# Kernel tuning notes

Measured on AMD Instinct MI355X. Metric: run time of the kernel, lower is better.

## Reference

```python
import jax, jax.numpy as jnp
import numpy as np

N_RAYS, N_SAMPLES, RES = 4096, 256, 128
RGB_C = 15
XYZ_MIN, XYZ_MAX = -1.0, 1.0
NEAR, FAR, STEPSIZE, BG = 0.2, 3.0, 0.5, 1.0
ALPHA_INIT = 0.01
ACT_SHIFT = float(np.log(1.0 / (1.0 - ALPHA_INIT) - 1.0))
N_FREQ = 6
EMB_DIM = 3 + 3 * 2 * N_FREQ  # 39
DIM0 = RGB_C + EMB_DIM        # 54


def _trilinear(grid, u):
    # grid: [C, R, R, R]; u: [N, 3] normalized to [0,1]; align_corners=True
    R = grid.shape[1]
    pos = jnp.clip(u, 0.0, 1.0) * (R - 1)
    i0 = jnp.clip(jnp.floor(pos).astype(jnp.int32), 0, R - 2)
    f = pos - i0.astype(pos.dtype)
    i1 = i0 + 1
    x0, y0, z0 = i0[:, 0], i0[:, 1], i0[:, 2]
    x1, y1, z1 = i1[:, 0], i1[:, 1], i1[:, 2]
    fx, fy, fz = f[:, 0], f[:, 1], f[:, 2]
    c = (grid[:, x0, y0, z0] * ((1 - fx) * (1 - fy) * (1 - fz))
         + grid[:, x1, y0, z0] * (fx * (1 - fy) * (1 - fz))
         + grid[:, x0, y1, z0] * ((1 - fx) * fy * (1 - fz))
         + grid[:, x0, y0, z1] * ((1 - fx) * (1 - fy) * fz)
         + grid[:, x1, y1, z0] * (fx * fy * (1 - fz))
         + grid[:, x1, y0, z1] * (fx * (1 - fy) * fz)
         + grid[:, x0, y1, z1] * ((1 - fx) * fy * fz)
         + grid[:, x1, y1, z1] * (fx * fy * fz))
    return c.T  # [N, C]


def _embed(x):
    # NeRF positional encoding, multires=6, include inputs: [..., 3] -> [..., 39]
    freqs = 2.0 ** jnp.arange(N_FREQ, dtype=x.dtype)
    xb = x[..., None, :] * freqs[:, None]  # [..., 6, 3]
    shp = x.shape[:-1]
    return jnp.concatenate([x, jnp.sin(xb).reshape(*shp, -1), jnp.cos(xb).reshape(*shp, -1)], -1)


def setup_inputs() -> dict:
    key = jax.random.key(0)
    ks = jax.random.split(key, 12)
    return {
        "rays_o": jax.random.uniform(ks[0], (N_RAYS, 3), minval=-0.5, maxval=0.5),
        "rays_d": jax.random.normal(ks[1], (N_RAYS, 3)),
        "viewdirs": jax.random.normal(ks[2], (N_RAYS, 3)),
        "latent_grid": jax.random.normal(ks[3], (1 + RGB_C, RES, RES, RES)) * 0.1,
        "normals_grid": jax.random.normal(ks[4], (3, RES, RES, RES)),
        "W0": jax.random.normal(ks[5], (DIM0, 64)) * 0.1, "b0": jnp.zeros((64,)),
        "W1": jax.random.normal(ks[6], (64, 64)) * 0.1, "b1": jnp.zeros((64,)),
        "W2": jax.random.normal(ks[7], (64, 64)) * 0.1, "b2": jnp.zeros((64,)),
        "W3": jax.random.normal(ks[8], (64, 3)) * 0.1, "b3": jnp.zeros((3,)),
    }


def reference(rays_o, rays_d, viewdirs, latent_grid, normals_grid,
              W0, b0, W1, b1, W2, b2, W3, b3):
    rays_d = rays_d / jnp.linalg.norm(rays_d, axis=-1, keepdims=True)
    viewdirs = viewdirs / jnp.linalg.norm(viewdirs, axis=-1, keepdims=True)
    # sample_ray: uniform steps along each ray
    t = jnp.linspace(NEAR, FAR, N_SAMPLES, dtype=rays_o.dtype)
    ray_pts = rays_o[:, None, :] + rays_d[:, None, :] * t[None, :, None]  # [R,S,3]
    inbbox = jnp.all((ray_pts >= XYZ_MIN) & (ray_pts <= XYZ_MAX), -1)      # [R,S]
    u = ((ray_pts - XYZ_MIN) / (XYZ_MAX - XYZ_MIN)).reshape(-1, 3)
    lat = _trilinear(latent_grid, u).reshape(N_RAYS, N_SAMPLES, 1 + RGB_C)
    nrm = _trilinear(normals_grid, u).reshape(N_RAYS, N_SAMPLES, 3)
    nrm = nrm / jnp.maximum(jnp.linalg.norm(nrm, axis=-1, keepdims=True), 1e-12)
    nrm = jnp.where(inbbox[..., None], nrm, 0.0)
    density = lat[..., 0]
    # activate_density: 1 - exp(-softplus(d + shift) * interval), zero outside bbox
    alpha = jnp.where(inbbox, 1.0 - jnp.exp(-jax.nn.softplus(density + ACT_SHIFT) * STEPSIZE), 0.0)
    # cumprod_exclusive transmittance
    alphainv_cum = jnp.concatenate(
        [jnp.ones_like(alpha[..., :1]), jnp.cumprod(jnp.clip(1.0 - alpha, 1e-10, None), -1)], -1)
    weights = alpha * alphainv_cum[..., :-1]
    # reflection directions: 2*(-v.n)*n + v
    vde = jnp.broadcast_to(viewdirs[:, None, :], nrm.shape)
    dot = jnp.sum(-vde * nrm, -1, keepdims=True)
    refdirs = 2.0 * dot * nrm + vde
    feat = jnp.concatenate([jnp.where(inbbox[..., None], lat[..., 1:], 0.0), _embed(refdirs)], -1)
    h = jax.nn.relu(feat @ W0 + b0)
    h = jax.nn.relu(h @ W1 + b1)
    h = jax.nn.relu(h @ W2 + b2)
    rgb = jnp.where(inbbox[..., None], jax.nn.sigmoid(h @ W3 + b3), 0.0)
    rgb_marched = jnp.sum(weights[..., None] * rgb, -2) + alphainv_cum[..., -1:] * BG
    depth = jnp.linalg.norm(rays_o[:, None, :] - ray_pts, axis=-1)
    depth_marched = jnp.sum(weights * depth, -1) + alphainv_cum[..., -1] * FAR
    disp = 1.0 / depth_marched
    acc = weights.sum(-1)
    normals_marched = jnp.sum(weights[..., None] * nrm, -2)
    return rgb_marched, depth_marched, disp, acc, normals_marched, weights, alphainv_cum
```

## Files before the change

kernel.cpp:

```cpp
#include <hip/hip_runtime.h>
#include <hip/hip_bf16.h>
#include <math.h>

typedef __hip_bfloat16 bf16;
typedef float f32x4 __attribute__((ext_vector_type(4)));
typedef short short8 __attribute__((ext_vector_type(8)));

#define NRAYS 4096
#define NSAMP 256
#define RESG  128
#define RS2   16384
#define RS3   2097152
#define ACT_SHIFT (-4.59511985013459f)

#define OFLAG 0
#define OBIAS 16
#define ORO   272
#define ORD   12560
#define OVD   24848
#define FRAG_BYTE_OFF 148544
#define LATIL_BYTE_OFF 1048576ULL
#define NRMIL_BYTE_OFF 68157440ULL
#define WS_NEED        101711872ULL

__device__ __forceinline__ float ldT(const float* p, size_t i){ return p[i]; }
__device__ __forceinline__ float ldT(const bf16*  p, size_t i){ return __bfloat162float(p[i]); }

__device__ __forceinline__ unsigned short f2bu(float f){
  unsigned int x = __float_as_uint(f);
  unsigned int r = (x + 0x7FFFu + ((x >> 16) & 1u)) >> 16;
  return (unsigned short)r;
}
__device__ __forceinline__ float bu2f(short s){
  return __uint_as_float(((unsigned int)(unsigned short)s) << 16);
}

template<typename T>
__device__ void fill_ws(const void* W0,const void* b0,const void* W1,const void* b1,
                        const void* W2,const void* b2,const void* W3,const void* b3,
                        const void* ro,const void* rd,const void* vd,
                        float* __restrict__ wb, int tid)
{
  const T* tW0=(const T*)W0; const T* tb0=(const T*)b0;
  const T* tW1=(const T*)W1; const T* tb1=(const T*)b1;
  const T* tW2=(const T*)W2; const T* tb2=(const T*)b2;
  const T* tW3=(const T*)W3; const T* tb3=(const T*)b3;
  const T* tro=(const T*)ro; const T* trd=(const T*)rd; const T* tvd=(const T*)vd;

  for (int idx = tid; idx < 64; idx += 256){
    wb[16+idx]  = ldT(tb0, idx);
    wb[80+idx]  = ldT(tb1, idx);
    wb[144+idx] = ldT(tb2, idx);
  }
  if (tid < 16) wb[224+tid] = (tid < 3) ? ldT(tb3, tid) : 0.0f;

  for (int r = tid; r < NRAYS; r += 256){
    float ox = ldT(tro, r*3+0), oy = ldT(tro, r*3+1), oz = ldT(tro, r*3+2);
    wb[ORO+r*3+0]=ox; wb[ORO+r*3+1]=oy; wb[ORO+r*3+2]=oz;
    float dx = ldT(trd, r*3+0), dy = ldT(trd, r*3+1), dz = ldT(trd, r*3+2);
    float dn = 1.0f / sqrtf(dx*dx+dy*dy+dz*dz);
    wb[ORD+r*3+0]=dx*dn; wb[ORD+r*3+1]=dy*dn; wb[ORD+r*3+2]=dz*dn;
    float vx = ldT(tvd, r*3+0), vy = ldT(tvd, r*3+1), vz = ldT(tvd, r*3+2);
    float vn = 1.0f / sqrtf(vx*vx+vy*vy+vz*vz);
    wb[OVD+r*3+0]=vx*vn; wb[OVD+r*3+1]=vy*vn; wb[OVD+r*3+2]=vz*vn;
  }

  unsigned short* fu = (unsigned short*)((char*)wb + FRAG_BYTE_OFF);
  for (int idx = tid; idx < 4096; idx += 256){
    int blk = idx >> 9, rem = idx & 511, lane = rem >> 3, j = rem & 7;
    int nt = blk >> 1, ks = blk & 1;
    int k = ks*32 + ((lane>>4)<<3) + j, n = nt*16 + (lane & 15);
    float v = (k < 54) ? ldT(tW0, k*64 + n) : 0.0f;
    fu[idx] = f2bu(v);
  }
  for (int idx = tid; idx < 4096; idx += 256){
    int blk = idx >> 9, rem = idx & 511, lane = rem >> 3, j = rem & 7;
    int nt = blk >> 1, ks = blk & 1;
    int k = ks*32 + ((lane>>4)<<3) + j, n = nt*16 + (lane & 15);
    fu[4096+idx] = f2bu(ldT(tW1, k*64 + n));
    fu[8192+idx] = f2bu(ldT(tW2, k*64 + n));
  }
  for (int idx = tid; idx < 1024; idx += 256){
    int blk = idx >> 9, rem = idx & 511, lane = rem >> 3, j = rem & 7;
    int ks = blk;
    int k = ks*32 + ((lane>>4)<<3) + j, n = lane & 15;
    float v = (n < 3) ? ldT(tW3, k*3 + n) : 0.0f;
    fu[12288+idx] = f2bu(v);
  }
}

__global__ void prep(const void* W0,const void* b0,const void* W1,const void* b1,
                     const void* W2,const void* b2,const void* W3,const void* b3,
                     const void* ro,const void* rd,const void* vd,
                     float* __restrict__ wb)
{
  __shared__ int s_f32;
  const int tid = threadIdx.x;
  if (tid == 0) s_f32 = 0;
  __syncthreads();
  {
    const bf16* t1 = (const bf16*)W1;
    float a = fabsf(__bfloat162float(t1[2*tid]));
    float b = fabsf(__bfloat162float(t1[2*tid+1]));
    if (!(a < 100.0f) || !(b < 100.0f)) atomicOr(&s_f32, 1);
  }
  __syncthreads();
  const bool isf32 = (s_f32 != 0);
  if (tid == 0) wb[OFLAG] = isf32 ? 1.0f : 0.0f;
  if (isf32) fill_ws<float>(W0,b0,W1,b1,W2,b2,W3,b3,ro,rd,vd,wb,tid);
  else       fill_ws<bf16 >(W0,b0,W1,b1,W2,b2,W3,b3,ro,rd,vd,wb,tid);
}

__global__ __launch_bounds__(256)
void interleave_lat(const void* __restrict__ latent, float* __restrict__ wb)
{
  unsigned short* lat_il = (unsigned short*)((char*)wb + LATIL_BYTE_OFF);
  const int T = blockIdx.x*256 + threadIdx.x;
  const int v = T >> 1, h = T & 1, cb = h*8;
  short8 o;
  if (wb[OFLAG] > 0.5f){
    const float* p = (const float*)latent;
#pragma unroll
    for (int j = 0; j < 8; j++) o[j] = (short)f2bu(p[(size_t)(cb+j)*RS3 + v]);
  } else {
    const unsigned short* p = (const unsigned short*)latent;
#pragma unroll
    for (int j = 0; j < 8; j++) o[j] = (short)p[(size_t)(cb+j)*RS3 + v];
  }
  *(short8*)&lat_il[((size_t)v<<4) + cb] = o;
}

__global__ __launch_bounds__(256)
void interleave_nrm(const void* __restrict__ normals, float* __restrict__ wb)
{
  f32x4* nrm_il = (f32x4*)((char*)wb + NRMIL_BYTE_OFF);
  const int v = blockIdx.x*256 + threadIdx.x;
  f32x4 o;
  if (wb[OFLAG] > 0.5f){
    const float* p = (const float*)normals;
    o[0]=p[v]; o[1]=p[(size_t)RS3+v]; o[2]=p[(size_t)2*RS3+v]; o[3]=0.0f;
  } else {
    const unsigned short* p = (const unsigned short*)normals;
    o[0]=bu2f(p[v]); o[1]=bu2f(p[(size_t)RS3+v]); o[2]=bu2f(p[(size_t)2*RS3+v]); o[3]=0.0f;
  }
  nrm_il[v] = o;
}

__global__ __launch_bounds__(256, 4)
void render_fast(const float* __restrict__ wb, float* __restrict__ out)
{
  const int ray  = blockIdx.x;
  const int i    = threadIdx.x;
  const int lane = i & 63;
  const int wv   = i >> 6;
  const int quad = lane >> 4;
  const int n15  = lane & 15;
  const int wbase = wv * 64;

  __shared__ unsigned short act[NSAMP*72];
  __shared__ float sh_w[NSAMP];
  __shared__ float sh_wt[4];
  __shared__ float red[4][8];
  __shared__ float red_rgb[4][16];

  const unsigned short* lat_il = (const unsigned short*)((const char*)wb + LATIL_BYTE_OFF);
  const f32x4* nrm_il = (const f32x4*)((const char*)wb + NRMIL_BYTE_OFF);

  const float ox = wb[ORO+ray*3+0], oy = wb[ORO+ray*3+1], oz = wb[ORO+ray*3+2];
  const float dx = wb[ORD+ray*3+0], dy = wb[ORD+ray*3+1], dz = wb[ORD+ray*3+2];
  const float vx = wb[OVD+ray*3+0], vy = wb[OVD+ray*3+1], vz = wb[OVD+ray*3+2];

  const float t  = 0.2f + (2.8f/255.0f) * (float)i;
  const float px = ox + dx*t, py = oy + dy*t, pz = oz + dz*t;
  const bool inb = (px >= -1.0f) & (px <= 1.0f) & (py >= -1.0f) & (py <= 1.0f)
                 & (pz >= -1.0f) & (pz <= 1.0f);

  float alpha = 0.0f, nx = 0.0f, ny = 0.0f, nz = 0.0f;
  unsigned short* arow = &act[i*72];

  if (inb) {
    float ux = fminf(fmaxf((px+1.0f)*0.5f, 0.0f), 1.0f) * 127.0f;
    float uy = fminf(fmaxf((py+1.0f)*0.5f, 0.0f), 1.0f) * 127.0f;
    float uz = fminf(fmaxf((pz+1.0f)*0.5f, 0.0f), 1.0f) * 127.0f;
    int x0 = (int)floorf(ux); x0 = x0 > 126 ? 126 : (x0 < 0 ? 0 : x0);
    int y0 = (int)floorf(uy); y0 = y0 > 126 ? 126 : (y0 < 0 ? 0 : y0);
    int z0 = (int)floorf(uz); z0 = z0 > 126 ? 126 : (z0 < 0 ? 0 : z0);
    float fx = ux - (float)x0, fy = uy - (float)y0, fz = uz - (float)z0;
    const float gx = 1.0f - fx, gy = 1.0f - fy, gz = 1.0f - fz;

    const int vb = (x0<<14) + (y0<<7) + z0;
    const unsigned short* Lp = lat_il + ((size_t)vb<<4);
    const f32x4* Np = nrm_il + vb;

    float ch[16];
#pragma unroll
    for (int c = 0; c < 16; c++) ch[c] = 0.0f;
    float nr0 = 0.0f, nr1 = 0.0f, nr2 = 0.0f;

    const int   loff[4] = {0, 1<<18, 1<<11, (1<<18)+(1<<11)};
    const int   noff[4] = {0, 16384, 128, 16384+128};
    const float wxy[4]  = {gx*gy, fx*gy, gx*fy, fx*fy};

#pragma unroll
    for (int cr = 0; cr < 4; cr++){
      const unsigned short* p = Lp + loff[cr];
      short8 a0 = *(const short8*)(p);
      short8 a1 = *(const short8*)(p+8);
      short8 b0 = *(const short8*)(p+16);
      short8 b1 = *(const short8*)(p+24);
      const float wz0 = wxy[cr]*gz, wz1 = wxy[cr]*fz;
#pragma unroll
      for (int j = 0; j < 8; j++){
        ch[j]   += wz0*bu2f(a0[j]) + wz1*bu2f(b0[j]);
        ch[j+8] += wz0*bu2f(a1[j]) + wz1*bu2f(b1[j]);
      }
      f32x4 n0 = Np[noff[cr]];
      f32x4 n1 = Np[noff[cr]+1];
      nr0 += wz0*n0[0] + wz1*n1[0];
      nr1 += wz0*n0[1] + wz1*n1[1];
      nr2 += wz0*n0[2] + wz1*n1[2];
    }

    float xs = ch[0] + ACT_SHIFT;
    float sp = xs > 15.0f ? xs : log1pf(__expf(xs));
    alpha = 1.0f - __expf(-sp * 0.5f);

    float nn  = sqrtf(nr0*nr0 + nr1*nr1 + nr2*nr2);
    float ninv = 1.0f / fmaxf(nn, 1e-12f);
    nx = nr0*ninv; ny = nr1*ninv; nz = nr2*ninv;

    float dt = -(vx*nx + vy*ny + vz*nz);
    float rx = 2.0f*dt*nx + vx, ry = 2.0f*dt*ny + vy, rz = 2.0f*dt*nz + vz;

    short8 v0, v1;
#pragma unroll
    for (int j = 0; j < 8; j++) v0[j] = (short)f2bu(ch[1+j]);
#pragma unroll
    for (int j = 0; j < 7; j++) v1[j] = (short)f2bu(ch[9+j]);
    v1[7] = (short)f2bu(rx);
    *(short8*)&arow[0] = v0; *(short8*)&arow[8] = v1;
    v0[0]=(short)f2bu(ry); v0[1]=(short)f2bu(rz);
    v0[2]=(short)f2bu(__sinf(rx));        v0[3]=(short)f2bu(__sinf(ry));        v0[4]=(short)f2bu(__sinf(rz));
    v0[5]=(short)f2bu(__sinf(rx*2.0f));   v0[6]=(short)f2bu(__sinf(ry*2.0f));   v0[7]=(short)f2bu(__sinf(rz*2.0f));
    v1[0]=(short)f2bu(__sinf(rx*4.0f));   v1[1]=(short)f2bu(__sinf(ry*4.0f));   v1[2]=(short)f2bu(__sinf(rz*4.0f));
    v1[3]=(short)f2bu(__sinf(rx*8.0f));   v1[4]=(short)f2bu(__sinf(ry*8.0f));   v1[5]=(short)f2bu(__sinf(rz*8.0f));
    v1[6]=(short)f2bu(__sinf(rx*16.0f));  v1[7]=(short)f2bu(__sinf(ry*16.0f));
    *(short8*)&arow[16] = v0; *(short8*)&arow[24] = v1;
    v0[0]=(short)f2bu(__sinf(rz*16.0f));  v0[1]=(short)f2bu(__sinf(rx*32.0f));
    v0[2]=(short)f2bu(__sinf(ry*32.0f));  v0[3]=(short)f2bu(__sinf(rz*32.0f));
    v0[4]=(short)f2bu(__cosf(rx));        v0[5]=(short)f2bu(__cosf(ry));        v0[6]=(short)f2bu(__cosf(rz));
    v0[7]=(short)f2bu(__cosf(rx*2.0f));
    v1[0]=(short)f2bu(__cosf(ry*2.0f));   v1[1]=(short)f2bu(__cosf(rz*2.0f));
    v1[2]=(short)f2bu(__cosf(rx*4.0f));   v1[3]=(short)f2bu(__cosf(ry*4.0f));   v1[4]=(short)f2bu(__cosf(rz*4.0f));
    v1[5]=(short)f2bu(__cosf(rx*8.0f));   v1[6]=(short)f2bu(__cosf(ry*8.0f));   v1[7]=(short)f2bu(__cosf(rz*8.0f));
    *(short8*)&arow[32] = v0; *(short8*)&arow[40] = v1;
    v0[0]=(short)f2bu(__cosf(rx*16.0f));  v0[1]=(short)f2bu(__cosf(ry*16.0f));  v0[2]=(short)f2bu(__cosf(rz*16.0f));
    v0[3]=(short)f2bu(__cosf(rx*32.0f));  v0[4]=(short)f2bu(__cosf(ry*32.0f));  v0[5]=(short)f2bu(__cosf(rz*32.0f));
    v0[6]=0; v0[7]=0;
#pragma unroll
    for (int j = 0; j < 8; j++) v1[j] = 0;
    *(short8*)&arow[48] = v0; *(short8*)&arow[56] = v1;
  } else {
    short8 z;
#pragma unroll
    for (int j = 0; j < 8; j++) z[j] = 0;
#pragma unroll
    for (int c = 0; c < 8; c++) *(short8*)&arow[c*8] = z;
  }

  float xv = fmaxf(1.0f - alpha, 1e-10f);
  float incl = xv;
#pragma unroll
  for (int off = 1; off < 64; off <<= 1){
    float y = __shfl_up(incl, off, 64);
    if (lane >= off) incl *= y;
  }
  float excl = __shfl_up(incl, 1, 64);
  if (lane == 0) excl = 1.0f;
  if (lane == 63) sh_wt[wv] = incl;
  __syncthreads();

  float pre = 1.0f;
#pragma unroll
  for (int k = 0; k < 4; k++) if (k < wv) pre *= sh_wt[k];
  const float last = sh_wt[0]*sh_wt[1]*sh_wt[2]*sh_wt[3];
  const float av = pre * excl;
  const float w  = alpha * av;
  sh_w[i] = w;

  float* outw = out + 36864;
  float* outa = out + 36864 + 1048576;
  outw[ray*NSAMP + i] = w;
  outa[ray*(NSAMP+1) + i] = av;
  if (i == NSAMP-1) outa[ray*(NSAMP+1) + NSAMP] = last;

  {
    float vals[5] = { w*t, w, w*nx, w*ny, w*nz };
#pragma unroll
    for (int v = 0; v < 5; v++){
      float s = vals[v];
#pragma unroll
      for (int m = 32; m > 0; m >>= 1) s += __shfl_xor(s, m, 64);
      if (lane == 0) red[wv][v] = s;
    }
  }
  __syncthreads();
  if (i == 0){
    float s0 = red[0][0]+red[1][0]+red[2][0]+red[3][0];
    float s1 = red[0][1]+red[1][1]+red[2][1]+red[3][1];
    float s2 = red[0][2]+red[1][2]+red[2][2]+red[3][2];
    float s3 = red[0][3]+red[1][3]+red[2][3]+red[3][3];
    float s4 = red[0][4]+red[1][4]+red[2][4]+red[3][4];
    const float dm = s0 + last * 3.0f;
    float* o1 = out + 12288; o1[ray] = dm;
    float* o2 = out + 16384; o2[ray] = 1.0f / dm;
    float* o3 = out + 20480; o3[ray] = s1;
    float* o4 = out + 24576;
    o4[ray*3+0] = s2; o4[ray*3+1] = s3; o4[ray*3+2] = s4;
  }

  const short8* fr = (const short8*)((const char*)wb + FRAG_BYTE_OFF);

#pragma unroll
  for (int l = 0; l < 3; l++){
    const int fbase = l * 512;
    f32x4 acc[4][4];
#pragma unroll
    for (int mt = 0; mt < 4; mt++)
#pragma unroll
      for (int nt = 0; nt < 4; nt++) acc[mt][nt] = (f32x4){0.f,0.f,0.f,0.f};

#pragma unroll
    for (int ks = 0; ks < 2; ks++){
      short8 a[4], b[4];
#pragma unroll
      for (int mt = 0; mt < 4; mt++)
        a[mt] = *(const short8*)&act[(wbase + mt*16 + n15)*72 + ks*32 + quad*8];
#pragma unroll
      for (int nt = 0; nt < 4; nt++)
        b[nt] = fr[fbase + (nt*2+ks)*64 + lane];
#pragma unroll
      for (int mt = 0; mt < 4; mt++)
#pragma unroll
        for (int nt = 0; nt < 4; nt++)
          acc[mt][nt] = __builtin_amdgcn_mfma_f32_16x16x32_bf16(a[mt], b[nt], acc[mt][nt], 0, 0, 0);
    }
    __syncthreads();
#pragma unroll
    for (int nt = 0; nt < 4; nt++){
      const float bn = wb[OBIAS + l*64 + nt*16 + n15];
#pragma unroll
      for (int mt = 0; mt < 4; mt++){
#pragma unroll
        for (int r = 0; r < 4; r++){
          float vv = fmaxf(acc[mt][nt][r] + bn, 0.0f);
          act[(wbase + mt*16 + quad*4 + r)*72 + nt*16 + n15] = f2bu(vv);
        }
      }
    }
    __syncthreads();
  }

  {
    f32x4 acc3[4];
#pragma unroll
    for (int mt = 0; mt < 4; mt++) acc3[mt] = (f32x4){0.f,0.f,0.f,0.f};
#pragma unroll
    for (int ks = 0; ks < 2; ks++){
      short8 a[4];
#pragma unroll
      for (int mt = 0; mt < 4; mt++)
        a[mt] = *(const short8*)&act[(wbase + mt*16 + n15)*72 + ks*32 + quad*8];
      short8 b = fr[1536 + ks*64 + lane];
#pragma unroll
      for (int mt = 0; mt < 4; mt++)
        acc3[mt] = __builtin_amdgcn_mfma_f32_16x16x32_bf16(a[mt], b, acc3[mt], 0, 0, 0);
    }
    const float bn3 = wb[OBIAS + 208 + n15];
    float p = 0.0f;
#pragma unroll
    for (int mt = 0; mt < 4; mt++){
#pragma unroll
      for (int r = 0; r < 4; r++){
        const float wr = sh_w[wbase + mt*16 + quad*4 + r];
        const float logit = acc3[mt][r] + bn3;
        p += wr * (1.0f / (1.0f + __expf(-logit)));
      }
    }
    p += __shfl_xor(p, 16, 64);
    p += __shfl_xor(p, 32, 64);
    if (lane < 16) red_rgb[wv][lane] = p;
  }
  __syncthreads();
  if (i < 3){
    float s = red_rgb[0][i] + red_rgb[1][i] + red_rgb[2][i] + red_rgb[3][i];
    out[ray*3+i] = s + last;
  }
}

template<typename GT>
__device__ __forceinline__ void render_body(const GT* __restrict__ latent,
                                            const GT* __restrict__ normals,
                                            const float* __restrict__ wb,
                                            float* __restrict__ out)
{
  const int ray  = blockIdx.x;
  const int i    = threadIdx.x;
  const int lane = i & 63;
  const int wv   = i >> 6;
  const int quad = lane >> 4;
  const int n15  = lane & 15;
  const int wbase = wv * 64;

  __shared__ unsigned short act[NSAMP*72];
  __shared__ float sh_w[NSAMP];
  __shared__ float sh_wt[4];
  __shared__ float red[4][8];
  __shared__ float red_rgb[4][16];

  const float ox = wb[ORO+ray*3+0], oy = wb[ORO+ray*3+1], oz = wb[ORO+ray*3+2];
  const float dx = wb[ORD+ray*3+0], dy = wb[ORD+ray*3+1], dz = wb[ORD+ray*3+2];
  const float vx = wb[OVD+ray*3+0], vy = wb[OVD+ray*3+1], vz = wb[OVD+ray*3+2];

  const float t  = 0.2f + (2.8f/255.0f) * (float)i;
  const float px = ox + dx*t, py = oy + dy*t, pz = oz + dz*t;
  const bool inb = (px >= -1.0f) & (px <= 1.0f) & (py >= -1.0f) & (py <= 1.0f)
                 & (pz >= -1.0f) & (pz <= 1.0f);

  float alpha = 0.0f, nx = 0.0f, ny = 0.0f, nz = 0.0f;
  float fv[64];
#pragma unroll
  for (int k = 0; k < 64; k++) fv[k] = 0.0f;

  if (inb) {
    float ux = fminf(fmaxf((px+1.0f)*0.5f, 0.0f), 1.0f) * 127.0f;
    float uy = fminf(fmaxf((py+1.0f)*0.5f, 0.0f), 1.0f) * 127.0f;
    float uz = fminf(fmaxf((pz+1.0f)*0.5f, 0.0f), 1.0f) * 127.0f;
    int x0 = (int)floorf(ux); x0 = x0 > 126 ? 126 : (x0 < 0 ? 0 : x0);
    int y0 = (int)floorf(uy); y0 = y0 > 126 ? 126 : (y0 < 0 ? 0 : y0);
    int z0 = (int)floorf(uz); z0 = z0 > 126 ? 126 : (z0 < 0 ? 0 : z0);
    float fx = ux - (float)x0, fy = uy - (float)y0, fz = uz - (float)z0;
    const int base = x0*RS2 + y0*RESG + z0;
    const float gx = 1.0f - fx, gy = 1.0f - fy, gz = 1.0f - fz;
    const float w000 = gx*gy*gz, w100 = fx*gy*gz, w010 = gx*fy*gz, w001 = gx*gy*fz;
    const float w110 = fx*fy*gz, w101 = fx*gy*fz, w011 = gx*fy*fz, w111 = fx*fy*fz;

    float ch[19];
#pragma unroll
    for (int c = 0; c < 19; c++){
      const GT* g = (c < 16 ? latent + c*RS3 : normals + (c-16)*RS3) + base;
      ch[c] = w000*ldT(g,0)        + w100*ldT(g,RS2)
            + w010*ldT(g,RESG)     + w001*ldT(g,1)
            + w110*ldT(g,RS2+RESG) + w101*ldT(g,RS2+1)
            + w011*ldT(g,RESG+1)   + w111*ldT(g,RS2+RESG+1);
    }

    float xs = ch[0] + ACT_SHIFT;
    float sp = xs > 15.0f ? xs : log1pf(__expf(xs));
    alpha = 1.0f - __expf(-sp * 0.5f);

    float nn  = sqrtf(ch[16]*ch[16] + ch[17]*ch[17] + ch[18]*ch[18]);
    float ninv = 1.0f / fmaxf(nn, 1e-12f);
    nx = ch[16]*ninv; ny = ch[17]*ninv; nz = ch[18]*ninv;

    float dt = -(vx*nx + vy*ny + vz*nz);
    float rx = 2.0f*dt*nx + vx, ry = 2.0f*dt*ny + vy, rz = 2.0f*dt*nz + vz;

#pragma unroll
    for (int k = 0; k < 15; k++) fv[k] = ch[k+1];
    fv[15] = rx; fv[16] = ry; fv[17] = rz;
#pragma unroll
    for (int f = 0; f < 6; f++){
      float s = (float)(1 << f);
      fv[18 + f*3 + 0] = __sinf(rx*s);
      fv[18 + f*3 + 1] = __sinf(ry*s);
      fv[18 + f*3 + 2] = __sinf(rz*s);
      fv[36 + f*3 + 0] = __cosf(rx*s);
      fv[36 + f*3 + 1] = __cosf(ry*s);
      fv[36 + f*3 + 2] = __cosf(rz*s);
    }
  }

#pragma unroll
  for (int c = 0; c < 8; c++){
    short8 v;
#pragma unroll
    for (int k = 0; k < 8; k++) v[k] = (short)f2bu(fv[c*8+k]);
    *(short8*)&act[i*72 + c*8] = v;
  }

  float xvv = fmaxf(1.0f - alpha, 1e-10f);
  float incl = xvv;
#pragma unroll
  for (int off = 1; off < 64; off <<= 1){
    float y = __shfl_up(incl, off, 64);
    if (lane >= off) incl *= y;
  }
  float excl = __shfl_up(incl, 1, 64);
  if (lane == 0) excl = 1.0f;
  if (lane == 63) sh_wt[wv] = incl;
  __syncthreads();

  float pre = 1.0f;
#pragma unroll
  for (int k = 0; k < 4; k++) if (k < wv) pre *= sh_wt[k];
  const float last = sh_wt[0]*sh_wt[1]*sh_wt[2]*sh_wt[3];
  const float av = pre * excl;
  const float w  = alpha * av;
  sh_w[i] = w;

  float* outw = out + 36864;
  float* outa = out + 36864 + 1048576;
  outw[ray*NSAMP + i] = w;
  outa[ray*(NSAMP+1) + i] = av;
  if (i == NSAMP-1) outa[ray*(NSAMP+1) + NSAMP] = last;

  {
    float vals[5] = { w*t, w, w*nx, w*ny, w*nz };
#pragma unroll
    for (int v = 0; v < 5; v++){
      float s = vals[v];
#pragma unroll
      for (int m = 32; m > 0; m >>= 1) s += __shfl_xor(s, m, 64);
      if (lane == 0) red[wv][v] = s;
    }
  }
  __syncthreads();
  if (i == 0){
    float s0 = red[0][0]+red[1][0]+red[2][0]+red[3][0];
    float s1 = red[0][1]+red[1][1]+red[2][1]+red[3][1];
    float s2 = red[0][2]+red[1][2]+red[2][2]+red[3][2];
    float s3 = red[0][3]+red[1][3]+red[2][3]+red[3][3];
    float s4 = red[0][4]+red[1][4]+red[2][4]+red[3][4];
    const float dm = s0 + last * 3.0f;
    float* o1 = out + 12288; o1[ray] = dm;
    float* o2 = out + 16384; o2[ray] = 1.0f / dm;
    float* o3 = out + 20480; o3[ray] = s1;
    float* o4 = out + 24576;
    o4[ray*3+0] = s2; o4[ray*3+1] = s3; o4[ray*3+2] = s4;
  }

  const short8* fr = (const short8*)((const char*)wb + FRAG_BYTE_OFF);

#pragma unroll
  for (int l = 0; l < 3; l++){
    const int fbase = l * 512;
    f32x4 acc[4][4];
#pragma unroll
    for (int mt = 0; mt < 4; mt++)
#pragma unroll
      for (int nt = 0; nt < 4; nt++) acc[mt][nt] = (f32x4){0.f,0.f,0.f,0.f};

#pragma unroll
    for (int ks = 0; ks < 2; ks++){
      short8 a[4], b[4];
#pragma unroll
      for (int mt = 0; mt < 4; mt++)
        a[mt] = *(const short8*)&act[(wbase + mt*16 + n15)*72 + ks*32 + quad*8];
#pragma unroll
      for (int nt = 0; nt < 4; nt++)
        b[nt] = fr[fbase + (nt*2+ks)*64 + lane];
#pragma unroll
      for (int mt = 0; mt < 4; mt++)
#pragma unroll
        for (int nt = 0; nt < 4; nt++)
          acc[mt][nt] = __builtin_amdgcn_mfma_f32_16x16x32_bf16(a[mt], b[nt], acc[mt][nt], 0, 0, 0);
    }
    __syncthreads();
#pragma unroll
    for (int nt = 0; nt < 4; nt++){
      const float bn = wb[OBIAS + l*64 + nt*16 + n15];
#pragma unroll
      for (int mt = 0; mt < 4; mt++){
#pragma unroll
        for (int r = 0; r < 4; r++){
          float vv = fmaxf(acc[mt][nt][r] + bn, 0.0f);
          act[(wbase + mt*16 + quad*4 + r)*72 + nt*16 + n15] = f2bu(vv);
        }
      }
    }
    __syncthreads();
  }

  {
    f32x4 acc3[4];
#pragma unroll
    for (int mt = 0; mt < 4; mt++) acc3[mt] = (f32x4){0.f,0.f,0.f,0.f};
#pragma unroll
    for (int ks = 0; ks < 2; ks++){
      short8 a[4];
#pragma unroll
      for (int mt = 0; mt < 4; mt++)
        a[mt] = *(const short8*)&act[(wbase + mt*16 + n15)*72 + ks*32 + quad*8];
      short8 b = fr[1536 + ks*64 + lane];
#pragma unroll
      for (int mt = 0; mt < 4; mt++)
        acc3[mt] = __builtin_amdgcn_mfma_f32_16x16x32_bf16(a[mt], b, acc3[mt], 0, 0, 0);
    }
    const float bn3 = wb[OBIAS + 208 + n15];
    float p = 0.0f;
#pragma unroll
    for (int mt = 0; mt < 4; mt++){
#pragma unroll
      for (int r = 0; r < 4; r++){
        const float wr = sh_w[wbase + mt*16 + quad*4 + r];
        const float logit = acc3[mt][r] + bn3;
        p += wr * (1.0f / (1.0f + __expf(-logit)));
      }
    }
    p += __shfl_xor(p, 16, 64);
    p += __shfl_xor(p, 32, 64);
    if (lane < 16) red_rgb[wv][lane] = p;
  }
  __syncthreads();
  if (i < 3){
    float s = red_rgb[0][i] + red_rgb[1][i] + red_rgb[2][i] + red_rgb[3][i];
    out[ray*3+i] = s + last;
  }
}

__global__ __launch_bounds__(256)
void render_fallback(const void* __restrict__ latent, const void* __restrict__ normals,
                     const float* __restrict__ wb, float* __restrict__ out)
{
  if (wb[OFLAG] > 0.5f)
    render_body<float>((const float*)latent, (const float*)normals, wb, out);
  else
    render_body<bf16 >((const bf16*)latent,  (const bf16*)normals,  wb, out);
}

extern "C" void kernel_launch(void* const* d_in, const int* in_sizes, int n_in,
                              void* d_out, int out_size, void* d_ws, size_t ws_size,
                              hipStream_t stream)
{
  float* wb = (float*)d_ws;
  prep<<<1, 256, 0, stream>>>(d_in[5], d_in[6], d_in[7], d_in[8],
                              d_in[9], d_in[10], d_in[11], d_in[12],
                              d_in[0], d_in[1], d_in[2], wb);
  if (ws_size >= WS_NEED){
    interleave_lat<<<16384, 256, 0, stream>>>(d_in[3], wb);
    interleave_nrm<<<8192, 256, 0, stream>>>(d_in[4], wb);
    render_fast<<<NRAYS, 256, 0, stream>>>(wb, (float*)d_out);
  } else {
    render_fallback<<<NRAYS, 256, 0, stream>>>(d_in[3], d_in[4], wb, (float*)d_out);
  }
}
```

Measured before the change: 362.1 us.

## Parallelize prep across blocks and fuse vectorized latent/normal interleave kernels

The single-block prep kernel is split across 53 blocks, each handling one slice of the weight-fragment, ray-normalization or bias work. The two grid-interleave kernels are merged into one launch, and each thread now handles 2 latent voxels or 4 normal voxels using vector loads and stores. This cuts serial prep latency, one kernel launch, and the number of narrow global memory transactions in the layout-conversion pass. Every block still re-runs the dtype detection, and the flag write now comes from only one block, which is safe only because later kernels run after prep finishes on the same stream.

```diff
diff --git a/kernel.cpp b/kernel.cpp
--- a/kernel.cpp
+++ b/kernel.cpp
@@ -4,7 +4,9 @@
 
 typedef __hip_bfloat16 bf16;
 typedef float f32x4 __attribute__((ext_vector_type(4)));
+typedef float f32x2 __attribute__((ext_vector_type(2)));
 typedef short short8 __attribute__((ext_vector_type(8)));
+typedef short short4v __attribute__((ext_vector_type(4)));
 
 #define NRAYS 4096
 #define NSAMP 256
@@ -35,11 +37,13 @@
   return __uint_as_float(((unsigned int)(unsigned short)s) << 16);
 }
 
+#define PREP_BLOCKS 53
+
 template<typename T>
-__device__ void fill_ws(const void* W0,const void* b0,const void* W1,const void* b1,
-                        const void* W2,const void* b2,const void* W3,const void* b3,
-                        const void* ro,const void* rd,const void* vd,
-                        float* __restrict__ wb, int tid)
+__device__ void fill_ws_part(const void* W0,const void* b0,const void* W1,const void* b1,
+                             const void* W2,const void* b2,const void* W3,const void* b3,
+                             const void* ro,const void* rd,const void* vd,
+                             float* __restrict__ wb, int bid, int tid, bool isf32)
 {
   const T* tW0=(const T*)W0; const T* tb0=(const T*)b0;
   const T* tW1=(const T*)W1; const T* tb1=(const T*)b1;
@@ -47,14 +51,10 @@
   const T* tW3=(const T*)W3; const T* tb3=(const T*)b3;
   const T* tro=(const T*)ro; const T* trd=(const T*)rd; const T* tvd=(const T*)vd;
 
-  for (int idx = tid; idx < 64; idx += 256){
-    wb[16+idx]  = ldT(tb0, idx);
-    wb[80+idx]  = ldT(tb1, idx);
-    wb[144+idx] = ldT(tb2, idx);
-  }
-  if (tid < 16) wb[224+tid] = (tid < 3) ? ldT(tb3, tid) : 0.0f;
-
-  for (int r = tid; r < NRAYS; r += 256){
+  unsigned short* fu = (unsigned short*)((char*)wb + FRAG_BYTE_OFF);
+
+  if (bid < 16){
+    const int r = bid*256 + tid;
     float ox = ldT(tro, r*3+0), oy = ldT(tro, r*3+1), oz = ldT(tro, r*3+2);
     wb[ORO+r*3+0]=ox; wb[ORO+r*3+1]=oy; wb[ORO+r*3+2]=oz;
     float dx = ldT(trd, r*3+0), dy = ldT(trd, r*3+1), dz = ldT(trd, r*3+2);
@@ -63,39 +63,47 @@
     float vx = ldT(tvd, r*3+0), vy = ldT(tvd, r*3+1), vz = ldT(tvd, r*3+2);
     float vn = 1.0f / sqrtf(vx*vx+vy*vy+vz*vz);
     wb[OVD+r*3+0]=vx*vn; wb[OVD+r*3+1]=vy*vn; wb[OVD+r*3+2]=vz*vn;
-  }
-
-  unsigned short* fu = (unsigned short*)((char*)wb + FRAG_BYTE_OFF);
-  for (int idx = tid; idx < 4096; idx += 256){
+  } else if (bid < 32){
+    const int idx = (bid-16)*256 + tid;
     int blk = idx >> 9, rem = idx & 511, lane = rem >> 3, j = rem & 7;
     int nt = blk >> 1, ks = blk & 1;
     int k = ks*32 + ((lane>>4)<<3) + j, n = nt*16 + (lane & 15);
     float v = (k < 54) ? ldT(tW0, k*64 + n) : 0.0f;
     fu[idx] = f2bu(v);
-  }
-  for (int idx = tid; idx < 4096; idx += 256){
+  } else if (bid < 48){
+    const int idx = (bid-32)*256 + tid;
     int blk = idx >> 9, rem = idx & 511, lane = rem >> 3, j = rem & 7;
     int nt = blk >> 1, ks = blk & 1;
     int k = ks*32 + ((lane>>4)<<3) + j, n = nt*16 + (lane & 15);
     fu[4096+idx] = f2bu(ldT(tW1, k*64 + n));
     fu[8192+idx] = f2bu(ldT(tW2, k*64 + n));
-  }
-  for (int idx = tid; idx < 1024; idx += 256){
+  } else if (bid < 52){
+    const int idx = (bid-48)*256 + tid;
     int blk = idx >> 9, rem = idx & 511, lane = rem >> 3, j = rem & 7;
     int ks = blk;
     int k = ks*32 + ((lane>>4)<<3) + j, n = lane & 15;
     float v = (n < 3) ? ldT(tW3, k*3 + n) : 0.0f;
     fu[12288+idx] = f2bu(v);
-  }
-}
-
-__global__ void prep(const void* W0,const void* b0,const void* W1,const void* b1,
-                     const void* W2,const void* b2,const void* W3,const void* b3,
-                     const void* ro,const void* rd,const void* vd,
-                     float* __restrict__ wb)
+  } else {
+    if (tid < 64){
+      wb[16+tid]  = ldT(tb0, tid);
+      wb[80+tid]  = ldT(tb1, tid);
+      wb[144+tid] = ldT(tb2, tid);
+    }
+    if (tid < 16) wb[224+tid] = (tid < 3) ? ldT(tb3, tid) : 0.0f;
+    if (tid == 0) wb[OFLAG] = isf32 ? 1.0f : 0.0f;
+  }
+}
+
+__global__ __launch_bounds__(256)
+void prep(const void* W0,const void* b0,const void* W1,const void* b1,
+          const void* W2,const void* b2,const void* W3,const void* b3,
+          const void* ro,const void* rd,const void* vd,
+          float* __restrict__ wb)
 {
   __shared__ int s_f32;
   const int tid = threadIdx.x;
+  const int bid = blockIdx.x;
   if (tid == 0) s_f32 = 0;
   __syncthreads();
   {
@@ -106,44 +114,69 @@
   }
   __syncthreads();
   const bool isf32 = (s_f32 != 0);
-  if (tid == 0) wb[OFLAG] = isf32 ? 1.0f : 0.0f;
-  if (isf32) fill_ws<float>(W0,b0,W1,b1,W2,b2,W3,b3,ro,rd,vd,wb,tid);
-  else       fill_ws<bf16 >(W0,b0,W1,b1,W2,b2,W3,b3,ro,rd,vd,wb,tid);
-}
+  if (isf32) fill_ws_part<float>(W0,b0,W1,b1,W2,b2,W3,b3,ro,rd,vd,wb,bid,tid,true);
+  else       fill_ws_part<bf16 >(W0,b0,W1,b1,W2,b2,W3,b3,ro,rd,vd,wb,bid,tid,false);
+}
+
+#define IL_BLOCKS 6144
 
 __global__ __launch_bounds__(256)
-void interleave_lat(const void* __restrict__ latent, float* __restrict__ wb)
+void interleave_all(const void* __restrict__ latent, const void* __restrict__ normals,
+                    float* __restrict__ wb)
 {
-  unsigned short* lat_il = (unsigned short*)((char*)wb + LATIL_BYTE_OFF);
-  const int T = blockIdx.x*256 + threadIdx.x;
-  const int v = T >> 1, h = T & 1, cb = h*8;
-  short8 o;
-  if (wb[OFLAG] > 0.5f){
-    const float* p = (const float*)latent;
-#pragma unroll
-    for (int j = 0; j < 8; j++) o[j] = (short)f2bu(p[(size_t)(cb+j)*RS3 + v]);
+  const bool isf32 = (wb[OFLAG] > 0.5f);
+  const int bid = blockIdx.x;
+  if (bid < 4096){
+    unsigned short* lat_il = (unsigned short*)((char*)wb + LATIL_BYTE_OFF);
+    const int v0 = (bid*256 + (int)threadIdx.x) * 2;
+    short8 o0a, o0b, o1a, o1b;
+    if (isf32){
+      const float* p = (const float*)latent;
+#pragma unroll
+      for (int c = 0; c < 8; c++){
+        f32x2 r0 = *(const f32x2*)&p[(size_t)c*RS3 + v0];
+        o0a[c] = (short)f2bu(r0[0]); o1a[c] = (short)f2bu(r0[1]);
+        f32x2 r1 = *(const f32x2*)&p[(size_t)(c+8)*RS3 + v0];
+        o0b[c] = (short)f2bu(r1[0]); o1b[c] = (short)f2bu(r1[1]);
+      }
+    } else {
+      const unsigned short* p = (const unsigned short*)latent;
+#pragma unroll
+      for (int c = 0; c < 8; c++){
+        unsigned int r0 = *(const unsigned int*)&p[(size_t)c*RS3 + v0];
+        o0a[c] = (short)(r0 & 0xFFFFu); o1a[c] = (short)(r0 >> 16);
+        unsigned int r1 = *(const unsigned int*)&p[(size_t)(c+8)*RS3 + v0];
+        o0b[c] = (short)(r1 & 0xFFFFu); o1b[c] = (short)(r1 >> 16);
+      }
+    }
+    unsigned short* q = &lat_il[(size_t)v0 << 4];
+    *(short8*)&q[0]  = o0a;
+    *(short8*)&q[8]  = o0b;
+    *(short8*)&q[16] = o1a;
+    *(short8*)&q[24] = o1b;
   } else {
-    const unsigned short* p = (const unsigned short*)latent;
-#pragma unroll
-    for (int j = 0; j < 8; j++) o[j] = (short)p[(size_t)(cb+j)*RS3 + v];
-  }
-  *(short8*)&lat_il[((size_t)v<<4) + cb] = o;
-}
-
-__global__ __launch_bounds__(256)
-void interleave_nrm(const void* __restrict__ normals, float* __restrict__ wb)
-{
-  f32x4* nrm_il = (f32x4*)((char*)wb + NRMIL_BYTE_OFF);
-  const int v = blockIdx.x*256 + threadIdx.x;
-  f32x4 o;
-  if (wb[OFLAG] > 0.5f){
-    const float* p = (const float*)normals;
-    o[0]=p[v]; o[1]=p[(size_t)RS3+v]; o[2]=p[(size_t)2*RS3+v]; o[3]=0.0f;
-  } else {
-    const unsigned short* p = (const unsigned short*)normals;
-    o[0]=bu2f(p[v]); o[1]=bu2f(p[(size_t)RS3+v]); o[2]=bu2f(p[(size_t)2*RS3+v]); o[3]=0.0f;
-  }
-  nrm_il[v] = o;
+    f32x4* nrm_il = (f32x4*)((char*)wb + NRMIL_BYTE_OFF);
+    const int v0 = ((bid-4096)*256 + (int)threadIdx.x) * 4;
+    f32x4 a, b, c;
+    if (isf32){
+      const float* p = (const float*)normals;
+      a = *(const f32x4*)&p[v0];
+      b = *(const f32x4*)&p[(size_t)RS3 + v0];
+      c = *(const f32x4*)&p[(size_t)2*RS3 + v0];
+    } else {
+      const unsigned short* p = (const unsigned short*)normals;
+      short4v sa = *(const short4v*)&p[v0];
+      short4v sb = *(const short4v*)&p[(size_t)RS3 + v0];
+      short4v sc = *(const short4v*)&p[(size_t)2*RS3 + v0];
+      a = (f32x4){bu2f(sa[0]), bu2f(sa[1]), bu2f(sa[2]), bu2f(sa[3])};
+      b = (f32x4){bu2f(sb[0]), bu2f(sb[1]), bu2f(sb[2]), bu2f(sb[3])};
+      c = (f32x4){bu2f(sc[0]), bu2f(sc[1]), bu2f(sc[2]), bu2f(sc[3])};
+    }
+#pragma unroll
+    for (int j = 0; j < 4; j++){
+      nrm_il[v0 + j] = (f32x4){a[j], b[j], c[j], 0.0f};
+    }
+  }
 }
 
 __global__ __launch_bounds__(256, 4)
@@ -634,12 +667,11 @@
                               hipStream_t stream)
 {
   float* wb = (float*)d_ws;
-  prep<<<1, 256, 0, stream>>>(d_in[5], d_in[6], d_in[7], d_in[8],
-                              d_in[9], d_in[10], d_in[11], d_in[12],
-                              d_in[0], d_in[1], d_in[2], wb);
+  prep<<<PREP_BLOCKS, 256, 0, stream>>>(d_in[5], d_in[6], d_in[7], d_in[8],
+                                        d_in[9], d_in[10], d_in[11], d_in[12],
+                                        d_in[0], d_in[1], d_in[2], wb);
   if (ws_size >= WS_NEED){
-    interleave_lat<<<16384, 256, 0, stream>>>(d_in[3], wb);
-    interleave_nrm<<<8192, 256, 0, stream>>>(d_in[4], wb);
+    interleave_all<<<IL_BLOCKS, 256, 0, stream>>>(d_in[3], d_in[4], wb);
     render_fast<<<NRAYS, 256, 0, stream>>>(wb, (float*)d_out);
   } else {
     render_fallback<<<NRAYS, 256, 0, stream>>>(d_in[3], d_in[4], wb, (float*)d_out);
```

Measured after the change: 347.2 us. 4.1% less time.
